# Optimization experiments

Measured on AMD Instinct MI355X. Metric: run time of the kernel, lower is better.

Reference implementation:

```python
import jax, jax.numpy as jnp
import numpy as np

B, T, I, H = 64, 512, 1024, 1024


def setup_inputs() -> dict:
    key = jax.random.key(0)
    k1, k2, k3, k4 = jax.random.split(key, 4)
    scale_ih = (6.0 / (H + I)) ** 0.5  # xavier_uniform bound
    scale_hh = (6.0 / (H + H)) ** 0.5
    return {
        "x": jax.random.normal(k1, (B, T, I), dtype=jnp.float32),
        "h0": jax.random.normal(k2, (1, B, H), dtype=jnp.float32),
        "W_ih": jax.random.uniform(k3, (H, I), dtype=jnp.float32, minval=-scale_ih, maxval=scale_ih),
        "b_ih": jnp.zeros((H,), dtype=jnp.float32),
        "W_hh": jax.random.uniform(k4, (H, H), dtype=jnp.float32, minval=-scale_hh, maxval=scale_hh),
        "b_hh": jnp.zeros((H,), dtype=jnp.float32),
    }


def reference(x, h0, W_ih, b_ih, W_hh, b_hh):
    # h_t = tanh(x_t @ W_ih^T + b_ih + h_{t-1} @ W_hh^T + b_hh)
    # Precompute the input projection for all timesteps (same math, batched GEMM).
    xp = jnp.einsum("bti,hi->tbh", x, W_ih) + b_ih  # [T,B,H]
    h = h0[0]  # [B,H]

    def step(h, xp_t):
        h_new = jnp.tanh(xp_t + h @ W_hh.T + b_hh)
        return h_new, h_new

    _, ys = jax.lax.scan(step, h, xp)  # ys: [T,B,H]
    return jnp.transpose(ys, (1, 0, 2))  # [B,T,H]
```

## Files before the change

### kernel.cpp

```cpp
#include <hip/hip_runtime.h>
#include <hip/hip_bf16.h>

#define BB_   64
#define TT_   512
#define II_   1024
#define HH_   1024

typedef _Float16 half8  __attribute__((ext_vector_type(8)));
typedef _Float16 half4v __attribute__((ext_vector_type(4)));
typedef float    f32x4  __attribute__((ext_vector_type(4)));

__device__ __forceinline__ float fast_tanh(float x) {
    float t = fminf(fmaxf(x, -16.f), 16.f);
    float e = __builtin_amdgcn_exp2f(t * 2.885390082f);
    return 1.f - 2.f * __builtin_amdgcn_rcpf(e + 1.f);
}

__global__ __launch_bounds__(256) void gemm_xp(const float* __restrict__ x,
                                               const float* __restrict__ Wih,
                                               const float* __restrict__ bih,
                                               float* __restrict__ out) {
    __shared__ alignas(16) _Float16 As[2][128 * 40];
    __shared__ alignas(16) _Float16 Bs[2][128 * 40];

    const int tid  = threadIdx.x;
    const int xcd  = blockIdx.x & 7;
    const int idx  = blockIdx.x >> 3;
    const int bm   = xcd + 8 * (idx >> 3);
    const int bn   = idx & 7;
    const int M0   = bm * 128, N0 = bn * 128;
    const int lane = tid & 63, w = tid >> 6;
    const int wm   = (w & 1) * 64, wn = (w >> 1) * 64;
    const int ro   = lane & 15, q = lane >> 4;
    const int sr   = tid >> 3, sc = tid & 7;

    const f32x4 zero4 = {0.f, 0.f, 0.f, 0.f};
    f32x4 acc[4][4];
    #pragma unroll
    for (int i = 0; i < 4; ++i)
        #pragma unroll
        for (int j = 0; j < 4; ++j) acc[i][j] = zero4;

    for (int kk = 0; kk < 16; ++kk) {
        #pragma unroll
        for (int sub = 0; sub < 2; ++sub) {
            const int k0 = kk * 64 + sub * 32;
            #pragma unroll
            for (int ir = 0; ir < 4; ++ir) {
                const int row = ir * 32 + sr;
                const float4 av = *(const float4*)(x   + (size_t)(M0 + row) * II_ + k0 + sc * 4);
                const float4 bv = *(const float4*)(Wih + (size_t)(N0 + row) * II_ + k0 + sc * 4);
                half4v ah = { (_Float16)av.x, (_Float16)av.y, (_Float16)av.z, (_Float16)av.w };
                half4v bh = { (_Float16)bv.x, (_Float16)bv.y, (_Float16)bv.z, (_Float16)bv.w };
                *(half4v*)(As[sub] + row * 40 + sc * 4) = ah;
                *(half4v*)(Bs[sub] + row * 40 + sc * 4) = bh;
            }
        }
        __syncthreads();

        half8 a[2][4], b[2][4];
        #pragma unroll
        for (int sub = 0; sub < 2; ++sub)
            #pragma unroll
            for (int i = 0; i < 4; ++i) {
                a[sub][i] = *(const half8*)(As[sub] + (wm + i * 16 + ro) * 40 + q * 8);
                b[sub][i] = *(const half8*)(Bs[sub] + (wn + i * 16 + ro) * 40 + q * 8);
            }
        #pragma unroll
        for (int sub = 0; sub < 2; ++sub)
            #pragma unroll
            for (int i = 0; i < 4; ++i)
                #pragma unroll
                for (int j = 0; j < 4; ++j)
                    acc[i][j] = __builtin_amdgcn_mfma_f32_16x16x32_f16(a[sub][i], b[sub][j], acc[i][j], 0, 0, 0);
        __syncthreads();
    }

    #pragma unroll
    for (int j = 0; j < 4; ++j) {
        const int col = N0 + wn + j * 16 + ro;
        const float bias = bih[col];
        #pragma unroll
        for (int i = 0; i < 4; ++i) {
            #pragma unroll
            for (int r = 0; r < 4; ++r) {
                const int rowg = M0 + wm + i * 16 + q * 4 + r;
                out[(size_t)rowg * HH_ + col] = acc[i][j][r] + bias;
            }
        }
    }
}

__global__ __launch_bounds__(256, 1) void rnn_steps(const float* __restrict__ Whh,
                                                    const float* __restrict__ bhh,
                                                    const float* __restrict__ h0,
                                                    float* __restrict__ out,
                                                    unsigned* __restrict__ comm) {
    __shared__ alignas(16) _Float16 hbuf[2][5][1032];

    const int tid  = threadIdx.x;
    const int lane = tid & 63;
    const int w    = tid >> 6;
    const int g    = blockIdx.x >> 4;
    const int wg   = blockIdx.x & 15;
    const int b0   = g * 4;
    const int j0   = wg * 64;
    const int ro   = lane & 15, q = lane >> 4;
    const int arow = (ro < 4) ? ro : 4;
    const int bat  = lane >> 4;
    const int colw = j0 + w * 16 + (lane & 15);

    half8 wf[4][8];
    {
        const float* wrow = Whh + (size_t)(j0 + w * 16 + ro) * HH_;
        #pragma unroll
        for (int kq = 0; kq < 4; ++kq) {
            #pragma unroll
            for (int ks = 0; ks < 8; ++ks) {
                const int kc = kq * 256 + ks * 32 + q * 8;
                const float4 w0 = *(const float4*)(wrow + kc);
                const float4 w1 = *(const float4*)(wrow + kc + 4);
                half8 hv;
                hv[0] = (_Float16)w0.x; hv[1] = (_Float16)w0.y;
                hv[2] = (_Float16)w0.z; hv[3] = (_Float16)w0.w;
                hv[4] = (_Float16)w1.x; hv[5] = (_Float16)w1.y;
                hv[6] = (_Float16)w1.z; hv[7] = (_Float16)w1.w;
                wf[kq][ks] = hv;
            }
        }
    }
    const float bhh_r = bhh[colw];

    for (int i = tid; i < 1032; i += 256) {
        hbuf[0][4][i] = (_Float16)0.f;
        hbuf[1][4][i] = (_Float16)0.f;
    }

    const f32x4 zero4 = {0.f, 0.f, 0.f, 0.f};

    #define TAGMSK_ 0xFFFF0000FFFF0000ull
    #define TAGOK_(v) ((((v) ^ pat) & TAGMSK_) == 0)

    for (int s = 0; s < TT_; ++s) {
        const int slot = s & 1;

        const float xpv = out[((size_t)(b0 + bat) * TT_ + s) * HH_ + colw];

        unsigned* dstw = (unsigned*)(&hbuf[slot][w][0]);
        if (s == 0) {
            const float2* hrow = (const float2*)(h0 + (size_t)(b0 + w) * HH_);
            #pragma unroll
            for (int c = 0; c < 8; ++c) {
                const float2 hv = hrow[c * 64 + lane];
                union { _Float16 h[2]; unsigned u; } pk;
                pk.h[0] = (_Float16)hv.x; pk.h[1] = (_Float16)hv.y;
                dstw[c * 64 + lane] = pk.u;
            }
        } else {
            const unsigned long long pat =
                ((unsigned long long)(unsigned)s << 48) |
                ((unsigned long long)(unsigned)s << 16);
            const unsigned long long* sp = (const unsigned long long*)
                (comm + (size_t)slot * (BB_ * HH_) + (size_t)(b0 + w) * HH_);
            unsigned long long v0, v1, v2, v3, v4, v5, v6, v7;
            bool ok = false;
            while (!ok) {
                v0 = __hip_atomic_load(sp + 0 * 64 + lane, __ATOMIC_RELAXED, __HIP_MEMORY_SCOPE_AGENT);
                v1 = __hip_atomic_load(sp + 1 * 64 + lane, __ATOMIC_RELAXED, __HIP_MEMORY_SCOPE_AGENT);
                v2 = __hip_atomic_load(sp + 2 * 64 + lane, __ATOMIC_RELAXED, __HIP_MEMORY_SCOPE_AGENT);
                v3 = __hip_atomic_load(sp + 3 * 64 + lane, __ATOMIC_RELAXED, __HIP_MEMORY_SCOPE_AGENT);
                v4 = __hip_atomic_load(sp + 4 * 64 + lane, __ATOMIC_RELAXED, __HIP_MEMORY_SCOPE_AGENT);
                v5 = __hip_atomic_load(sp + 5 * 64 + lane, __ATOMIC_RELAXED, __HIP_MEMORY_SCOPE_AGENT);
                v6 = __hip_atomic_load(sp + 6 * 64 + lane, __ATOMIC_RELAXED, __HIP_MEMORY_SCOPE_AGENT);
                v7 = __hip_atomic_load(sp + 7 * 64 + lane, __ATOMIC_RELAXED, __HIP_MEMORY_SCOPE_AGENT);
                bool o = true;
                o &= TAGOK_(v0); o &= TAGOK_(v1); o &= TAGOK_(v2); o &= TAGOK_(v3);
                o &= TAGOK_(v4); o &= TAGOK_(v5); o &= TAGOK_(v6); o &= TAGOK_(v7);
                ok = o;
            }
            #define PACK_(x) ((unsigned)((x) & 0xffffull) | (((unsigned)((x) >> 32)) << 16))
            dstw[0 * 64 + lane] = PACK_(v0);
            dstw[1 * 64 + lane] = PACK_(v1);
            dstw[2 * 64 + lane] = PACK_(v2);
            dstw[3 * 64 + lane] = PACK_(v3);
            dstw[4 * 64 + lane] = PACK_(v4);
            dstw[5 * 64 + lane] = PACK_(v5);
            dstw[6 * 64 + lane] = PACK_(v6);
            dstw[7 * 64 + lane] = PACK_(v7);
            #undef PACK_
        }
        __syncthreads();

        f32x4 acc[4] = {zero4, zero4, zero4, zero4};
        const _Float16* abase = &hbuf[slot][0][0] + (size_t)arow * 1032;
        #pragma unroll
        for (int kq = 0; kq < 4; ++kq) {
            #pragma unroll
            for (int ks = 0; ks < 8; ++ks) {
                const half8 a = *(const half8*)(abase + kq * 256 + ks * 32 + q * 8);
                acc[kq] = __builtin_amdgcn_mfma_f32_16x16x32_f16(a, wf[kq][ks], acc[kq], 0, 0, 0);
            }
        }

        const f32x4 sum = acc[0] + acc[1] + acc[2] + acc[3];
        const float t0 = __shfl(sum[0], lane & 15);
        const float t1 = __shfl(sum[1], lane & 15);
        const float t2 = __shfl(sum[2], lane & 15);
        const float t3 = __shfl(sum[3], lane & 15);
        const float val = (bat == 0) ? t0 : (bat == 1) ? t1 : (bat == 2) ? t2 : t3;

        const float hnew = fast_tanh(xpv + bhh_r + val);

        union { _Float16 h; unsigned short us; } cv; cv.h = (_Float16)hnew;
        const unsigned word = ((unsigned)(s + 1) << 16) | (unsigned)cv.us;
        __hip_atomic_store(comm + (size_t)((s + 1) & 1) * (BB_ * HH_)
                                + (size_t)(b0 + bat) * HH_ + colw,
                           word, __ATOMIC_RELAXED, __HIP_MEMORY_SCOPE_AGENT);

        out[((size_t)(b0 + bat) * TT_ + s) * HH_ + colw] = hnew;
    }
    #undef TAGOK_
    #undef TAGMSK_
}

extern "C" void kernel_launch(void* const* d_in, const int* in_sizes, int n_in,
                              void* d_out, int out_size, void* d_ws, size_t ws_size,
                              hipStream_t stream) {
    (void)in_sizes; (void)n_in; (void)out_size; (void)ws_size;

    const float* x   = (const float*)d_in[0];
    const float* h0  = (const float*)d_in[1];
    const float* Wih = (const float*)d_in[2];
    const float* bih = (const float*)d_in[3];
    const float* Whh = (const float*)d_in[4];
    const float* bhh = (const float*)d_in[5];
    float* out = (float*)d_out;

    unsigned* comm = (unsigned*)d_ws;

    gemm_xp<<<2048, 256, 0, stream>>>(x, Wih, bih, out);
    rnn_steps<<<256, 256, 0, stream>>>(Whh, bhh, h0, out, comm);
}
```

Before: 1.462 ms.

## Pre-convert x and W_ih to fp16 and software-pipeline the spin-wait polling

```diff
diff --git a/kernel.cpp b/kernel.cpp
--- a/kernel.cpp
+++ b/kernel.cpp
@@ -14,6 +14,87 @@
     float t = fminf(fmaxf(x, -16.f), 16.f);
     float e = __builtin_amdgcn_exp2f(t * 2.885390082f);
     return 1.f - 2.f * __builtin_amdgcn_rcpf(e + 1.f);
+}
+
+__global__ __launch_bounds__(256) void cvt_f16(const float4* __restrict__ src,
+                                               half4v* __restrict__ dst, int n4) {
+    int i = blockIdx.x * blockDim.x + threadIdx.x;
+    const int stride = gridDim.x * blockDim.x;
+    for (; i < n4; i += stride) {
+        const float4 v = src[i];
+        half4v h = { (_Float16)v.x, (_Float16)v.y, (_Float16)v.z, (_Float16)v.w };
+        dst[i] = h;
+    }
+}
+
+__global__ __launch_bounds__(256) void gemm_xp_f16(const _Float16* __restrict__ xh,
+                                                   const _Float16* __restrict__ Wh,
+                                                   const float* __restrict__ bih,
+                                                   float* __restrict__ out) {
+    __shared__ alignas(16) _Float16 As[128 * 72];
+    __shared__ alignas(16) _Float16 Bs[128 * 72];
+
+    const int tid  = threadIdx.x;
+    const int xcd  = blockIdx.x & 7;
+    const int idx  = blockIdx.x >> 3;
+    const int bm   = xcd + 8 * (idx >> 3);
+    const int bn   = idx & 7;
+    const int M0   = bm * 128, N0 = bn * 128;
+    const int lane = tid & 63, w = tid >> 6;
+    const int wm   = (w & 1) * 64, wn = (w >> 1) * 64;
+    const int ro   = lane & 15, q = lane >> 4;
+    const int sr   = tid >> 3, sc = tid & 7;
+
+    const f32x4 zero4 = {0.f, 0.f, 0.f, 0.f};
+    f32x4 acc[4][4];
+    #pragma unroll
+    for (int i = 0; i < 4; ++i)
+        #pragma unroll
+        for (int j = 0; j < 4; ++j) acc[i][j] = zero4;
+
+    for (int kk = 0; kk < 16; ++kk) {
+        const int k0 = kk * 64;
+        #pragma unroll
+        for (int ir = 0; ir < 4; ++ir) {
+            const int row = ir * 32 + sr;
+            const half8 av = *(const half8*)(xh + (size_t)(M0 + row) * II_ + k0 + sc * 8);
+            const half8 bv = *(const half8*)(Wh + (size_t)(N0 + row) * II_ + k0 + sc * 8);
+            *(half8*)(As + row * 72 + sc * 8) = av;
+            *(half8*)(Bs + row * 72 + sc * 8) = bv;
+        }
+        __syncthreads();
+
+        half8 a[2][4], b[2][4];
+        #pragma unroll
+        for (int sub = 0; sub < 2; ++sub)
+            #pragma unroll
+            for (int i = 0; i < 4; ++i) {
+                a[sub][i] = *(const half8*)(As + (wm + i * 16 + ro) * 72 + sub * 32 + q * 8);
+                b[sub][i] = *(const half8*)(Bs + (wn + i * 16 + ro) * 72 + sub * 32 + q * 8);
+            }
+        #pragma unroll
+        for (int sub = 0; sub < 2; ++sub)
+            #pragma unroll
+            for (int i = 0; i < 4; ++i)
+                #pragma unroll
+                for (int j = 0; j < 4; ++j)
+                    acc[i][j] = __builtin_amdgcn_mfma_f32_16x16x32_f16(a[sub][i], b[sub][j], acc[i][j], 0, 0, 0);
+        __syncthreads();
+    }
+
+    #pragma unroll
+    for (int j = 0; j < 4; ++j) {
+        const int col = N0 + wn + j * 16 + ro;
+        const float bias = bih[col];
+        #pragma unroll
+        for (int i = 0; i < 4; ++i) {
+            #pragma unroll
+            for (int r = 0; r < 4; ++r) {
+                const int rowg = M0 + wm + i * 16 + q * 4 + r;
+                out[(size_t)rowg * HH_ + col] = acc[i][j][r] + bias;
+            }
+        }
+    }
 }
 
 __global__ __launch_bounds__(256) void gemm_xp(const float* __restrict__ x,
@@ -140,6 +221,7 @@
 
     #define TAGMSK_ 0xFFFF0000FFFF0000ull
     #define TAGOK_(v) ((((v) ^ pat) & TAGMSK_) == 0)
+    #define AL_(p) __hip_atomic_load((p), __ATOMIC_RELAXED, __HIP_MEMORY_SCOPE_AGENT)
 
     for (int s = 0; s < TT_; ++s) {
         const int slot = s & 1;
@@ -162,22 +244,44 @@
                 ((unsigned long long)(unsigned)s << 16);
             const unsigned long long* sp = (const unsigned long long*)
                 (comm + (size_t)slot * (BB_ * HH_) + (size_t)(b0 + w) * HH_);
-            unsigned long long v0, v1, v2, v3, v4, v5, v6, v7;
-            bool ok = false;
-            while (!ok) {
-                v0 = __hip_atomic_load(sp + 0 * 64 + lane, __ATOMIC_RELAXED, __HIP_MEMORY_SCOPE_AGENT);
-                v1 = __hip_atomic_load(sp + 1 * 64 + lane, __ATOMIC_RELAXED, __HIP_MEMORY_SCOPE_AGENT);
-                v2 = __hip_atomic_load(sp + 2 * 64 + lane, __ATOMIC_RELAXED, __HIP_MEMORY_SCOPE_AGENT);
-                v3 = __hip_atomic_load(sp + 3 * 64 + lane, __ATOMIC_RELAXED, __HIP_MEMORY_SCOPE_AGENT);
-                v4 = __hip_atomic_load(sp + 4 * 64 + lane, __ATOMIC_RELAXED, __HIP_MEMORY_SCOPE_AGENT);
-                v5 = __hip_atomic_load(sp + 5 * 64 + lane, __ATOMIC_RELAXED, __HIP_MEMORY_SCOPE_AGENT);
-                v6 = __hip_atomic_load(sp + 6 * 64 + lane, __ATOMIC_RELAXED, __HIP_MEMORY_SCOPE_AGENT);
-                v7 = __hip_atomic_load(sp + 7 * 64 + lane, __ATOMIC_RELAXED, __HIP_MEMORY_SCOPE_AGENT);
-                bool o = true;
-                o &= TAGOK_(v0); o &= TAGOK_(v1); o &= TAGOK_(v2); o &= TAGOK_(v3);
-                o &= TAGOK_(v4); o &= TAGOK_(v5); o &= TAGOK_(v6); o &= TAGOK_(v7);
-                ok = o;
-            }
+
+            unsigned long long a0, a1, a2, a3, a4, a5, a6, a7;
+            unsigned long long c0, c1, c2, c3, c4, c5, c6, c7;
+            bool sel;
+            a0 = AL_(sp + 0 * 64 + lane); a1 = AL_(sp + 1 * 64 + lane);
+            a2 = AL_(sp + 2 * 64 + lane); a3 = AL_(sp + 3 * 64 + lane);
+            a4 = AL_(sp + 4 * 64 + lane); a5 = AL_(sp + 5 * 64 + lane);
+            a6 = AL_(sp + 6 * 64 + lane); a7 = AL_(sp + 7 * 64 + lane);
+            for (;;) {
+                c0 = AL_(sp + 0 * 64 + lane); c1 = AL_(sp + 1 * 64 + lane);
+                c2 = AL_(sp + 2 * 64 + lane); c3 = AL_(sp + 3 * 64 + lane);
+                c4 = AL_(sp + 4 * 64 + lane); c5 = AL_(sp + 5 * 64 + lane);
+                c6 = AL_(sp + 6 * 64 + lane); c7 = AL_(sp + 7 * 64 + lane);
+                {
+                    bool o = true;
+                    o &= TAGOK_(a0); o &= TAGOK_(a1); o &= TAGOK_(a2); o &= TAGOK_(a3);
+                    o &= TAGOK_(a4); o &= TAGOK_(a5); o &= TAGOK_(a6); o &= TAGOK_(a7);
+                    if (o) { sel = true; break; }
+                }
+                a0 = AL_(sp + 0 * 64 + lane); a1 = AL_(sp + 1 * 64 + lane);
+                a2 = AL_(sp + 2 * 64 + lane); a3 = AL_(sp + 3 * 64 + lane);
+                a4 = AL_(sp + 4 * 64 + lane); a5 = AL_(sp + 5 * 64 + lane);
+                a6 = AL_(sp + 6 * 64 + lane); a7 = AL_(sp + 7 * 64 + lane);
+                {
+                    bool o = true;
+                    o &= TAGOK_(c0); o &= TAGOK_(c1); o &= TAGOK_(c2); o &= TAGOK_(c3);
+                    o &= TAGOK_(c4); o &= TAGOK_(c5); o &= TAGOK_(c6); o &= TAGOK_(c7);
+                    if (o) { sel = false; break; }
+                }
+            }
+            const unsigned long long v0 = sel ? a0 : c0;
+            const unsigned long long v1 = sel ? a1 : c1;
+            const unsigned long long v2 = sel ? a2 : c2;
+            const unsigned long long v3 = sel ? a3 : c3;
+            const unsigned long long v4 = sel ? a4 : c4;
+            const unsigned long long v5 = sel ? a5 : c5;
+            const unsigned long long v6 = sel ? a6 : c6;
+            const unsigned long long v7 = sel ? a7 : c7;
             #define PACK_(x) ((unsigned)((x) & 0xffffull) | (((unsigned)((x) >> 32)) << 16))
             dstw[0 * 64 + lane] = PACK_(v0);
             dstw[1 * 64 + lane] = PACK_(v1);
@@ -221,12 +325,13 @@
     }
     #undef TAGOK_
     #undef TAGMSK_
+    #undef AL_
 }
 
 extern "C" void kernel_launch(void* const* d_in, const int* in_sizes, int n_in,
                               void* d_out, int out_size, void* d_ws, size_t ws_size,
                               hipStream_t stream) {
-    (void)in_sizes; (void)n_in; (void)out_size; (void)ws_size;
+    (void)in_sizes; (void)n_in; (void)out_size;
 
     const float* x   = (const float*)d_in[0];
     const float* h0  = (const float*)d_in[1];
@@ -236,8 +341,21 @@
     const float* bhh = (const float*)d_in[5];
     float* out = (float*)d_out;
 
+    const size_t COMMB = 2 * (size_t)(BB_ * HH_) * sizeof(unsigned);
+    const size_t WFB   = (size_t)HH_ * II_ * sizeof(_Float16);
+    const size_t XFB   = (size_t)BB_ * TT_ * II_ * sizeof(_Float16);
     unsigned* comm = (unsigned*)d_ws;
 
-    gemm_xp<<<2048, 256, 0, stream>>>(x, Wih, bih, out);
+    if (ws_size >= COMMB + WFB + XFB) {
+        _Float16* Wh = (_Float16*)((char*)d_ws + COMMB);
+        _Float16* xh = (_Float16*)((char*)d_ws + COMMB + WFB);
+        cvt_f16<<<512, 256, 0, stream>>>((const float4*)Wih, (half4v*)Wh,
+                                         HH_ * II_ / 4);
+        cvt_f16<<<2048, 256, 0, stream>>>((const float4*)x, (half4v*)xh,
+                                          BB_ * TT_ * II_ / 4);
+        gemm_xp_f16<<<2048, 256, 0, stream>>>(xh, Wh, bih, out);
+    } else {
+        gemm_xp<<<2048, 256, 0, stream>>>(x, Wih, bih, out);
+    }
     rnn_steps<<<256, 256, 0, stream>>>(Whh, bhh, h0, out, comm);
 }
```

After: 1.469 ms. Within noise of the previous version (+0.5%).
